# Kernel optimization log

Measured on AMD Instinct MI355X. Metric: run time of the kernel, lower is better.

Reference implementation:

```python
import jax, jax.numpy as jnp
import numpy as np
from math import factorial, sqrt

# (mul, l) lists after e3nn normalization/mul-splitting (muls already aligned)
RS1 = [(256, 0), (256, 1), (256, 2)]
RS2 = [(256, 1), (256, 1), (256, 2)]


def _su2_cg(j1, m1, j2, m2, j3, m3):
    # Racah formula for SU(2) Clebsch-Gordan <j1 m1 j2 m2 | j3 m3> (e3nn convention)
    if m3 != m1 + m2:
        return 0.0
    vmin = max(-j1 + j2 + m3, -j1 + m1, 0)
    vmax = min(j2 + j3 + m1, j3 - j1 + j2, j3 + m3)
    f = factorial
    C = sqrt((2 * j3 + 1)
             * f(j3 + j1 - j2) * f(j3 - j1 + j2) * f(j1 + j2 - j3) * f(j3 + m3) * f(j3 - m3)
             / (f(j1 + j2 + j3 + 1) * f(j1 - m1) * f(j1 + m1) * f(j2 - m2) * f(j2 + m2)))
    S = 0.0
    for v in range(vmin, vmax + 1):
        S += (-1.0) ** (v + j2 + m2) * (f(j2 + j3 + m1 - v) * f(j1 - m1 + v)
             / (f(v) * f(j3 - j1 + j2 - v) * f(j3 + m3 - v) * f(v + j1 - j2 - m3)))
    return C * S


def _su2_cg_tensor(j1, j2, j3):
    mat = np.zeros((2 * j1 + 1, 2 * j2 + 1, 2 * j3 + 1))
    for m1 in range(-j1, j1 + 1):
        for m2 in range(-j2, j2 + 1):
            m3 = m1 + m2
            if abs(m3) <= j3:
                mat[j1 + m1, j2 + m2, j3 + m3] = _su2_cg(j1, m1, j2, m2, j3, m3)
    return mat / sqrt(2 * j3 + 1)  # Wigner-3j normalization


def _q(l):
    # change of basis real -> complex spherical harmonics (e3nn convention)
    q = np.zeros((2 * l + 1, 2 * l + 1), dtype=np.complex128)
    for m in range(-l, 0):
        q[l + m, l + abs(m)] = 1.0 / sqrt(2)
        q[l + m, l - abs(m)] = -1j / sqrt(2)
    q[l, l] = 1.0
    for m in range(1, l + 1):
        q[l + m, l + abs(m)] = (-1) ** m / sqrt(2)
        q[l + m, l - abs(m)] = 1j * (-1) ** m / sqrt(2)
    return (-1j) ** l * q


def _wigner3j(l1, l2, l3):
    # real-basis Wigner 3j tensor, shape (2l1+1, 2l2+1, 2l3+1)
    C = _su2_cg_tensor(l1, l2, l3)
    Q1, Q2, Q3 = _q(l1), _q(l2), _q(l3)
    C = np.einsum('ij,kl,nm,ikn->jlm', Q1, Q2, np.conj(Q3), C)
    assert np.abs(C.imag).max() < 1e-6
    return C.real


# precomputed CG blocks C[(l, l1, l2)] of shape (2l+1, 2l1+1, 2l2+1), scaled by sqrt(2l+1)
CG = {}
for (_mul1, _l1), (_mul2, _l2) in zip(RS1, RS2):
    if _l1 != 0 and _l2 != 0:
        for _l in range(abs(_l1 - _l2), _l1 + _l2 + 1):
            CG[(_l, _l1, _l2)] = jnp.asarray(_wigner3j(_l, _l1, _l2) * sqrt(2 * _l + 1), dtype=jnp.float32)


def _forward(features_1, features_2):
    size = features_1.shape[:-1]
    f1 = features_1.reshape(-1, features_1.shape[-1])
    f2 = features_2.reshape(-1, features_2.shape[-1])
    B = f1.shape[0]
    out, i1, i2 = [], 0, 0
    for (mul, l1), (_, l2) in zip(RS1, RS2):
        d1, d2 = 2 * l1 + 1, 2 * l2 + 1
        x1 = f1[:, i1:i1 + mul * d1].reshape(B, mul, d1)
        i1 += mul * d1
        x2 = f2[:, i2:i2 + mul * d2].reshape(B, mul, d2)
        i2 += mul * d2
        if l1 == 0 or l2 == 0:
            # CG with a scalar is (a multiple of) identity -> elementwise product
            out.append((x1 * x2).reshape(B, -1))
        else:
            for l in range(abs(l1 - l2), l1 + l2 + 1):
                C = CG[(l, l1, l2)]  # (2l+1, d1, d2)
                out.append(jnp.einsum('ijk,bmj,bmk->bmi', C, x1, x2).reshape(B, -1))
    return jnp.concatenate(out, axis=1).reshape(*size, -1)


def setup_inputs() -> dict:
    key = jax.random.key(0)
    k1, k2 = jax.random.split(key)
    n1 = sum(m * (2 * l + 1) for m, l in RS1)  # 2304
    n2 = sum(m * (2 * l + 1) for m, l in RS2)  # 2816
    B = 8192
    return {
        'features_1': jax.random.normal(k1, (B, n1), dtype=jnp.float32),
        'features_2': jax.random.normal(k2, (B, n2), dtype=jnp.float32),
    }


def reference(features_1, features_2):
    return _forward(features_1, features_2)
```

## Files before the change

### kernel.cpp

```cpp
#include <hip/hip_runtime.h>

namespace cg {

constexpr double fact(int n) {
  double r = 1.0;
  for (int i = 2; i <= n; ++i) r *= (double)i;
  return r;
}

constexpr double csqrt(double x) {
  if (x <= 0.0) return 0.0;
  double g = x < 1.0 ? 1.0 : x;
  for (int i = 0; i < 80; ++i) g = 0.5 * (g + x / g);
  return g;
}

struct cplx { double re, im; };
constexpr cplx cmul(cplx a, cplx b) {
  return cplx{a.re * b.re - a.im * b.im, a.re * b.im + a.im * b.re};
}

constexpr double su2_cg(int j1, int m1, int j2, int m2, int j3, int m3) {
  if (m3 != m1 + m2) return 0.0;
  int vmin = -j1 + j2 + m3;
  if (-j1 + m1 > vmin) vmin = -j1 + m1;
  if (0 > vmin) vmin = 0;
  int vmax = j2 + j3 + m1;
  if (j3 - j1 + j2 < vmax) vmax = j3 - j1 + j2;
  if (j3 + m3 < vmax) vmax = j3 + m3;
  const double C = csqrt((2.0 * j3 + 1.0)
      * fact(j3 + j1 - j2) * fact(j3 - j1 + j2) * fact(j1 + j2 - j3)
      * fact(j3 + m3) * fact(j3 - m3)
      / (fact(j1 + j2 + j3 + 1) * fact(j1 - m1) * fact(j1 + m1)
         * fact(j2 - m2) * fact(j2 + m2)));
  double S = 0.0;
  for (int v = vmin; v <= vmax; ++v) {
    const double sgn = ((v + j2 + m2) & 1) ? -1.0 : 1.0;
    S += sgn * (fact(j2 + j3 + m1 - v) * fact(j1 - m1 + v)
         / (fact(v) * fact(j3 - j1 + j2 - v) * fact(j3 + m3 - v)
            * fact(v + j1 - j2 - m3)));
  }
  return C * S;
}

template <int L> struct QMat { cplx q[2 * L + 1][2 * L + 1]; };

template <int L>
constexpr QMat<L> make_q() {
  QMat<L> Q{};
  const double s = 1.0 / csqrt(2.0);
  for (int m = -L; m < 0; ++m) {
    Q.q[L + m][L - m] = cplx{s, 0.0};
    Q.q[L + m][L + m] = cplx{0.0, -s};
  }
  Q.q[L][L] = cplx{1.0, 0.0};
  for (int m = 1; m <= L; ++m) {
    const double sg = (m & 1) ? -1.0 : 1.0;
    Q.q[L + m][L + m] = cplx{sg * s, 0.0};
    Q.q[L + m][L - m] = cplx{0.0, sg * s};
  }
  cplx p{1.0, 0.0};
  for (int t = 0; t < L; ++t) p = cmul(p, cplx{0.0, -1.0});
  for (int r = 0; r < 2 * L + 1; ++r)
    for (int c = 0; c < 2 * L + 1; ++c)
      Q.q[r][c] = cmul(p, Q.q[r][c]);
  return Q;
}

template <int L, int L1, int L2>
struct W3 { float t[2 * L + 1][2 * L1 + 1][2 * L2 + 1]; };

template <int L, int L1, int L2>
constexpr W3<L, L1, L2> wigner() {
  const QMat<L>  Q1 = make_q<L>();
  const QMat<L1> Q2 = make_q<L1>();
  const QMat<L2> Q3 = make_q<L2>();
  double C[2 * L + 1][2 * L1 + 1][2 * L2 + 1] = {};
  for (int m1 = -L; m1 <= L; ++m1)
    for (int m2 = -L1; m2 <= L1; ++m2) {
      const int m3 = m1 + m2;
      if (m3 >= -L2 && m3 <= L2)
        C[L + m1][L1 + m2][L2 + m3] = su2_cg(L, m1, L1, m2, L2, m3);
    }
  const double scale = csqrt(2.0 * L + 1.0) / csqrt(2.0 * L2 + 1.0);
  W3<L, L1, L2> R{};
  for (int j = 0; j < 2 * L + 1; ++j)
    for (int l = 0; l < 2 * L1 + 1; ++l)
      for (int m = 0; m < 2 * L2 + 1; ++m) {
        cplx acc{0.0, 0.0};
        for (int i = 0; i < 2 * L + 1; ++i) {
          const cplx q1 = Q1.q[i][j];
          if (q1.re == 0.0 && q1.im == 0.0) continue;
          for (int k = 0; k < 2 * L1 + 1; ++k) {
            const cplx q2 = Q2.q[k][l];
            if (q2.re == 0.0 && q2.im == 0.0) continue;
            const cplx q12 = cmul(q1, q2);
            for (int n = 0; n < 2 * L2 + 1; ++n) {
              const double c = C[i][k][n];
              if (c == 0.0) continue;
              const cplx q3c{Q3.q[n][m].re, -Q3.q[n][m].im};
              const cplx term = cmul(q12, q3c);
              acc.re += term.re * c;
              acc.im += term.im * c;
            }
          }
        }
        R.t[j][l][m] = (float)(acc.re * scale);
      }
  return R;
}

constexpr W3<0, 1, 1> W011 = wigner<0, 1, 1>();
constexpr W3<1, 1, 1> W111 = wigner<1, 1, 1>();
constexpr W3<2, 1, 1> W211 = wigner<2, 1, 1>();
constexpr W3<0, 2, 2> W022 = wigner<0, 2, 2>();
constexpr W3<1, 2, 2> W122 = wigner<1, 2, 2>();
constexpr W3<2, 2, 2> W222 = wigner<2, 2, 2>();
constexpr W3<3, 2, 2> W322 = wigner<3, 2, 2>();
constexpr W3<4, 2, 2> W422 = wigner<4, 2, 2>();

}


template <int L, int L1, int L2>
__device__ __forceinline__ void contract(const cg::W3<L, L1, L2>& W,
                                         const float (&p)[2 * L1 + 1][2 * L2 + 1],
                                         float (&o)[2 * L + 1]) {
#pragma unroll
  for (int i = 0; i < 2 * L + 1; ++i) {
    float acc = 0.0f;
#pragma unroll
    for (int j = 0; j < 2 * L1 + 1; ++j)
#pragma unroll
      for (int k = 0; k < 2 * L2 + 1; ++k) {
        const float c = W.t[i][j][k];
        if (c != 0.0f) acc = __builtin_fmaf(c, p[j][k], acc);
      }
    o[i] = acc;
  }
}

__global__ __launch_bounds__(256) void tp_kernel(
    const float* __restrict__ f1, const float* __restrict__ f2,
    float* __restrict__ out, int B) {
  const int b = blockIdx.x;
  if (b >= B) return;
  const int m = threadIdx.x;
  const float* F1 = f1 + (size_t)b * 2304;
  const float* F2 = f2 + (size_t)b * 2816;
  float* O = out + (size_t)b * 9472;

  {
    const float s = F1[m];
#pragma unroll
    for (int k = 0; k < 3; ++k) O[m * 3 + k] = s * F2[m * 3 + k];
  }

  {
    float a[3], c[3];
#pragma unroll
    for (int j = 0; j < 3; ++j) a[j] = F1[256 + m * 3 + j];
#pragma unroll
    for (int k = 0; k < 3; ++k) c[k] = F2[768 + m * 3 + k];
    float p[3][3];
#pragma unroll
    for (int j = 0; j < 3; ++j)
#pragma unroll
      for (int k = 0; k < 3; ++k) p[j][k] = a[j] * c[k];
    float o0[1], o1[3], o2[5];
    contract<0, 1, 1>(cg::W011, p, o0);
    contract<1, 1, 1>(cg::W111, p, o1);
    contract<2, 1, 1>(cg::W211, p, o2);
    O[768 + m] = o0[0];
#pragma unroll
    for (int i = 0; i < 3; ++i) O[1024 + m * 3 + i] = o1[i];
#pragma unroll
    for (int i = 0; i < 5; ++i) O[1792 + m * 5 + i] = o2[i];
  }

  {
    float a[5], c[5];
#pragma unroll
    for (int j = 0; j < 5; ++j) a[j] = F1[1024 + m * 5 + j];
#pragma unroll
    for (int k = 0; k < 5; ++k) c[k] = F2[1536 + m * 5 + k];
    float p[5][5];
#pragma unroll
    for (int j = 0; j < 5; ++j)
#pragma unroll
      for (int k = 0; k < 5; ++k) p[j][k] = a[j] * c[k];
    float q0[1], q1[3], q2[5], q3[7], q4[9];
    contract<0, 2, 2>(cg::W022, p, q0);
    contract<1, 2, 2>(cg::W122, p, q1);
    contract<2, 2, 2>(cg::W222, p, q2);
    contract<3, 2, 2>(cg::W322, p, q3);
    contract<4, 2, 2>(cg::W422, p, q4);
    O[3072 + m] = q0[0];
#pragma unroll
    for (int i = 0; i < 3; ++i) O[3328 + m * 3 + i] = q1[i];
#pragma unroll
    for (int i = 0; i < 5; ++i) O[4096 + m * 5 + i] = q2[i];
#pragma unroll
    for (int i = 0; i < 7; ++i) O[5376 + m * 7 + i] = q3[i];
#pragma unroll
    for (int i = 0; i < 9; ++i) O[7168 + m * 9 + i] = q4[i];
  }
}

extern "C" void kernel_launch(void* const* d_in, const int* in_sizes, int n_in,
                              void* d_out, int out_size, void* d_ws, size_t ws_size,
                              hipStream_t stream) {
  const float* f1 = (const float*)d_in[0];
  const float* f2 = (const float*)d_in[1];
  float* out = (float*)d_out;
  const int B = in_sizes[0] / 2304;
  tp_kernel<<<B, 256, 0, stream>>>(f1, f2, out, B);
}
```

Measured before the change: 104.0 us.

## Stage inputs and outputs through LDS for coalesced float4 global access

Loads each row's two input feature vectors into shared memory with coalesced float4 reads, computes the tensor products from LDS, then writes results to LDS and copies them to global memory as coalesced float4 stores. This replaces strided per-thread global accesses (stride 3/5/7/9 floats) with fully coalesced vector transactions. It adds about 37 KB of LDS per block plus extra barriers, which may limit occupancy.

```diff
diff --git a/kernel.cpp b/kernel.cpp
--- a/kernel.cpp
+++ b/kernel.cpp
@@ -125,7 +125,7 @@
 template <int L, int L1, int L2>
 __device__ __forceinline__ void contract(const cg::W3<L, L1, L2>& W,
                                          const float (&p)[2 * L1 + 1][2 * L2 + 1],
-                                         float (&o)[2 * L + 1]) {
+                                         float* __restrict__ o) {
 #pragma unroll
   for (int i = 0; i < 2 * L + 1; ++i) {
     float acc = 0.0f;
@@ -143,67 +143,91 @@
 __global__ __launch_bounds__(256) void tp_kernel(
     const float* __restrict__ f1, const float* __restrict__ f2,
     float* __restrict__ out, int B) {
+  __shared__ __align__(16) float lds[9472];
   const int b = blockIdx.x;
   if (b >= B) return;
-  const int m = threadIdx.x;
-  const float* F1 = f1 + (size_t)b * 2304;
-  const float* F2 = f2 + (size_t)b * 2816;
-  float* O = out + (size_t)b * 9472;
-
-  {
-    const float s = F1[m];
-#pragma unroll
-    for (int k = 0; k < 3; ++k) O[m * 3 + k] = s * F2[m * 3 + k];
-  }
-
+  const int t = threadIdx.x;
+
+  {
+    const float4* s1 = reinterpret_cast<const float4*>(f1 + (size_t)b * 2304);
+    const float4* s2 = reinterpret_cast<const float4*>(f2 + (size_t)b * 2816);
+    float4* l4 = reinterpret_cast<float4*>(lds);
+#pragma unroll
+    for (int k = 0; k < 2; ++k) l4[t + k * 256] = s1[t + k * 256];
+    if (t < 64) l4[512 + t] = s1[512 + t];
+#pragma unroll
+    for (int k = 0; k < 2; ++k) l4[576 + t + k * 256] = s2[t + k * 256];
+    if (t < 192) l4[1088 + t] = s2[512 + t];
+  }
+  __syncthreads();
+
+  const int m = t;
+  float r0[3];
+  float o0, o1[3], o2[5];
+  float q0, q1[3], q2[5], q3[7], q4[9];
+  {
+    const float s = lds[m];
+#pragma unroll
+    for (int k = 0; k < 3; ++k) r0[k] = s * lds[2304 + m * 3 + k];
+  }
   {
     float a[3], c[3];
 #pragma unroll
-    for (int j = 0; j < 3; ++j) a[j] = F1[256 + m * 3 + j];
-#pragma unroll
-    for (int k = 0; k < 3; ++k) c[k] = F2[768 + m * 3 + k];
+    for (int j = 0; j < 3; ++j) a[j] = lds[256 + m * 3 + j];
+#pragma unroll
+    for (int k = 0; k < 3; ++k) c[k] = lds[2304 + 768 + m * 3 + k];
     float p[3][3];
 #pragma unroll
     for (int j = 0; j < 3; ++j)
 #pragma unroll
       for (int k = 0; k < 3; ++k) p[j][k] = a[j] * c[k];
-    float o0[1], o1[3], o2[5];
-    contract<0, 1, 1>(cg::W011, p, o0);
+    contract<0, 1, 1>(cg::W011, p, &o0);
     contract<1, 1, 1>(cg::W111, p, o1);
     contract<2, 1, 1>(cg::W211, p, o2);
-    O[768 + m] = o0[0];
-#pragma unroll
-    for (int i = 0; i < 3; ++i) O[1024 + m * 3 + i] = o1[i];
-#pragma unroll
-    for (int i = 0; i < 5; ++i) O[1792 + m * 5 + i] = o2[i];
-  }
-
+  }
   {
     float a[5], c[5];
 #pragma unroll
-    for (int j = 0; j < 5; ++j) a[j] = F1[1024 + m * 5 + j];
-#pragma unroll
-    for (int k = 0; k < 5; ++k) c[k] = F2[1536 + m * 5 + k];
+    for (int j = 0; j < 5; ++j) a[j] = lds[1024 + m * 5 + j];
+#pragma unroll
+    for (int k = 0; k < 5; ++k) c[k] = lds[2304 + 1536 + m * 5 + k];
     float p[5][5];
 #pragma unroll
     for (int j = 0; j < 5; ++j)
 #pragma unroll
       for (int k = 0; k < 5; ++k) p[j][k] = a[j] * c[k];
-    float q0[1], q1[3], q2[5], q3[7], q4[9];
-    contract<0, 2, 2>(cg::W022, p, q0);
+    contract<0, 2, 2>(cg::W022, p, &q0);
     contract<1, 2, 2>(cg::W122, p, q1);
     contract<2, 2, 2>(cg::W222, p, q2);
     contract<3, 2, 2>(cg::W322, p, q3);
     contract<4, 2, 2>(cg::W422, p, q4);
-    O[3072 + m] = q0[0];
-#pragma unroll
-    for (int i = 0; i < 3; ++i) O[3328 + m * 3 + i] = q1[i];
-#pragma unroll
-    for (int i = 0; i < 5; ++i) O[4096 + m * 5 + i] = q2[i];
-#pragma unroll
-    for (int i = 0; i < 7; ++i) O[5376 + m * 7 + i] = q3[i];
-#pragma unroll
-    for (int i = 0; i < 9; ++i) O[7168 + m * 9 + i] = q4[i];
+  }
+  __syncthreads();
+
+#pragma unroll
+  for (int k = 0; k < 3; ++k) lds[m * 3 + k] = r0[k];
+  lds[768 + m] = o0;
+#pragma unroll
+  for (int i = 0; i < 3; ++i) lds[1024 + m * 3 + i] = o1[i];
+#pragma unroll
+  for (int i = 0; i < 5; ++i) lds[1792 + m * 5 + i] = o2[i];
+  lds[3072 + m] = q0;
+#pragma unroll
+  for (int i = 0; i < 3; ++i) lds[3328 + m * 3 + i] = q1[i];
+#pragma unroll
+  for (int i = 0; i < 5; ++i) lds[4096 + m * 5 + i] = q2[i];
+#pragma unroll
+  for (int i = 0; i < 7; ++i) lds[5376 + m * 7 + i] = q3[i];
+#pragma unroll
+  for (int i = 0; i < 9; ++i) lds[7168 + m * 9 + i] = q4[i];
+  __syncthreads();
+
+  {
+    const float4* l4 = reinterpret_cast<const float4*>(lds);
+    float4* dst = reinterpret_cast<float4*>(out + (size_t)b * 9472);
+#pragma unroll
+    for (int k = 0; k < 9; ++k) dst[t + k * 256] = l4[t + k * 256];
+    if (t < 64) dst[2304 + t] = l4[2304 + t];
   }
 }
 
```

Measured after the change: 94.67 us. 1.1x faster.
